# Kernel tuning notes

Hardware: AMD Instinct MI355X
Metric: run time of the kernel (lower is better)

The kernel has to match this reference:

```python
import jax, jax.numpy as jnp
import numpy as np

NUM_NODES = 50000
NUM_EDGES = 800000
IN_DIM = 128
OUT_DIM = 128


def setup_inputs() -> dict:
    key = jax.random.key(0)
    k1, k2, k3 = jax.random.split(key, 3)
    x = jax.random.normal(k1, (NUM_NODES, IN_DIM), dtype=jnp.float32)
    edge_index = jax.random.randint(k2, (2, NUM_EDGES), 0, NUM_NODES, dtype=jnp.int64)
    # xavier_uniform-like init
    limit = float(np.sqrt(6.0 / (IN_DIM + OUT_DIM)))
    weight = jax.random.uniform(k3, (IN_DIM, OUT_DIM), minval=-limit, maxval=limit, dtype=jnp.float32)
    bias = jnp.zeros((OUT_DIM,), dtype=jnp.float32)
    return {"x": x, "edge_index": edge_index, "weight": weight, "bias": bias}


def reference(x, edge_index, weight, bias):
    num_nodes = x.shape[0]
    # add self loops
    self_loops = jnp.broadcast_to(jnp.arange(num_nodes, dtype=edge_index.dtype)[None, :], (2, num_nodes))
    ei = jnp.concatenate([edge_index, self_loops], axis=1)  # [2, E+N]
    row, col = ei[0], ei[1]

    transformed = x @ weight  # [N, out_dim]

    # symmetric normalization: deg counted over source indices (row), as in original
    deg = jax.ops.segment_sum(jnp.ones_like(row, dtype=x.dtype), row, num_segments=num_nodes)
    deg_inv_sqrt = jnp.where(deg > 0, deg ** -0.5, 0.0)
    norm = deg_inv_sqrt[row] * deg_inv_sqrt[col]  # [E+N]

    # gather-scale-scatter: out[dst] += norm * transformed[src]
    messages = norm[:, None] * transformed[row]  # [E+N, out_dim]
    out = jax.ops.segment_sum(messages, col, num_segments=num_nodes)
    return out + bias
```

## Files before the change

### kernel.cpp

```cpp
#include <hip/hip_runtime.h>
#include <hip/hip_fp16.h>


#define EPB 4096

typedef _Float16 f16;
typedef f16 f16x8 __attribute__((ext_vector_type(8)));
typedef float f32x4 __attribute__((ext_vector_type(4)));

static inline int cdiv(int a, int b) { return (a + b - 1) / b; }

__global__ __launch_bounds__(256) void k_hist(const int* __restrict__ ei, int E,
                                              int* __restrict__ hist, int nblk, int nbins,
                                              const float* __restrict__ W,
                                              f16* __restrict__ WhT) {
  __shared__ int ha[256], hb[256];
  const int tid = threadIdx.x, blk = blockIdx.x;
  ha[tid] = 0; hb[tid] = 0;
  __syncthreads();
  const int base = blk * EPB;
  const int lim = min(EPB, E - base);
  if ((E & 3) == 0) {
    for (int i = tid * 4; i + 3 < lim; i += 1024) {
      int4 s4 = *(const int4*)(ei + base + i);
      int4 d4 = *(const int4*)(ei + E + base + i);
      atomicAdd(&ha[d4.x >> 8], 1); atomicAdd(&hb[s4.x >> 8], 1);
      atomicAdd(&ha[d4.y >> 8], 1); atomicAdd(&hb[s4.y >> 8], 1);
      atomicAdd(&ha[d4.z >> 8], 1); atomicAdd(&hb[s4.z >> 8], 1);
      atomicAdd(&ha[d4.w >> 8], 1); atomicAdd(&hb[s4.w >> 8], 1);
    }
    for (int i = (lim & ~3) + tid; i < lim; i += 256) {
      atomicAdd(&ha[ei[E + base + i] >> 8], 1);
      atomicAdd(&hb[ei[base + i] >> 8], 1);
    }
  } else {
    for (int i = tid; i < lim; i += 256) {
      atomicAdd(&ha[ei[E + base + i] >> 8], 1);
      atomicAdd(&hb[ei[base + i] >> 8], 1);
    }
  }
  if (blk < 64) {
    int i = blk * 256 + tid;
    int k = i >> 7, c = i & 127;
    WhT[c * 128 + k] = (f16)W[i];
  }
  __syncthreads();
  if (tid < nbins) {
    hist[tid * nblk + blk] = ha[tid];
    hist[nbins * nblk + tid * nblk + blk] = hb[tid];
  }
}

__global__ __launch_bounds__(256) void k_scan1(int* __restrict__ a,
                                               int* __restrict__ partials, int M) {
  __shared__ int ws[256];
  const int tid = threadIdx.x;
  const int i0 = blockIdx.x * 1024 + tid * 4;
  int v0 = (i0 + 0 < M) ? a[i0 + 0] : 0;
  int v1 = (i0 + 1 < M) ? a[i0 + 1] : 0;
  int v2 = (i0 + 2 < M) ? a[i0 + 2] : 0;
  int v3 = (i0 + 3 < M) ? a[i0 + 3] : 0;
  int tsum = v0 + v1 + v2 + v3;
  ws[tid] = tsum;
  __syncthreads();
#pragma unroll
  for (int off = 1; off < 256; off <<= 1) {
    int add = (tid >= off) ? ws[tid - off] : 0;
    __syncthreads();
    ws[tid] += add;
    __syncthreads();
  }
  int texcl = ws[tid] - tsum;
  if (tid == 255) partials[blockIdx.x] = ws[255];
  if (i0 + 0 < M) a[i0 + 0] = texcl;
  if (i0 + 1 < M) a[i0 + 1] = texcl + v0;
  if (i0 + 2 < M) a[i0 + 2] = texcl + v0 + v1;
  if (i0 + 3 < M) a[i0 + 3] = texcl + v0 + v1 + v2;
}

__device__ __forceinline__ void scan_partials(const int* __restrict__ partials,
                                              int nb1, int* shP, int tid) {
  int v = (tid < nb1) ? partials[tid] : 0;
  shP[tid] = v;
  __syncthreads();
#pragma unroll
  for (int off = 1; off < 256; off <<= 1) {
    int add = (tid >= off) ? shP[tid - off] : 0;
    __syncthreads();
    shP[tid] += add;
    __syncthreads();
  }
  int excl = shP[tid] - v;
  __syncthreads();
  shP[tid] = excl;
  __syncthreads();
}

__global__ __launch_bounds__(256) void k_part(const int* __restrict__ ei, int E,
                                              const int* __restrict__ hist,
                                              const int* __restrict__ partials, int nb1,
                                              int nblk, int nbins,
                                              int* __restrict__ ebA,
                                              unsigned char* __restrict__ ebB) {
  __shared__ int cA[256], cB[256], shP[256];
  const int tid = threadIdx.x, blk = blockIdx.x;
  const int HALF = nbins * nblk;
  scan_partials(partials, nb1, shP, tid);
  if (tid < nbins) {
    int ia = tid * nblk + blk;
    int ib = HALF + tid * nblk + blk;
    cA[tid] = hist[ia] + shP[ia >> 10];
    cB[tid] = hist[ib] + shP[ib >> 10] - E;
  }
  __syncthreads();
  const int base = blk * EPB;
  const int lim = min(EPB, E - base);
  if ((E & 3) == 0) {
    for (int i = tid * 4; i + 3 < lim; i += 1024) {
      int4 s4 = *(const int4*)(ei + base + i);
      int4 d4 = *(const int4*)(ei + E + base + i);
      int pa, pb;
      pa = atomicAdd(&cA[d4.x >> 8], 1); ebA[pa] = (s4.x << 8) | (d4.x & 255);
      pb = atomicAdd(&cB[s4.x >> 8], 1); ebB[pb] = (unsigned char)(s4.x & 255);
      pa = atomicAdd(&cA[d4.y >> 8], 1); ebA[pa] = (s4.y << 8) | (d4.y & 255);
      pb = atomicAdd(&cB[s4.y >> 8], 1); ebB[pb] = (unsigned char)(s4.y & 255);
      pa = atomicAdd(&cA[d4.z >> 8], 1); ebA[pa] = (s4.z << 8) | (d4.z & 255);
      pb = atomicAdd(&cB[s4.z >> 8], 1); ebB[pb] = (unsigned char)(s4.z & 255);
      pa = atomicAdd(&cA[d4.w >> 8], 1); ebA[pa] = (s4.w << 8) | (d4.w & 255);
      pb = atomicAdd(&cB[s4.w >> 8], 1); ebB[pb] = (unsigned char)(s4.w & 255);
    }
    for (int i = (lim & ~3) + tid; i < lim; i += 256) {
      int s = ei[base + i], d = ei[E + base + i];
      int pa = atomicAdd(&cA[d >> 8], 1); ebA[pa] = (s << 8) | (d & 255);
      int pb = atomicAdd(&cB[s >> 8], 1); ebB[pb] = (unsigned char)(s & 255);
    }
  } else {
    for (int i = tid; i < lim; i += 256) {
      int s = ei[base + i], d = ei[E + base + i];
      int pa = atomicAdd(&cA[d >> 8], 1); ebA[pa] = (s << 8) | (d & 255);
      int pb = atomicAdd(&cB[s >> 8], 1); ebB[pb] = (unsigned char)(s & 255);
    }
  }
}

__global__ __launch_bounds__(256) void k_bucket(
    const int* __restrict__ ebA, const unsigned char* __restrict__ ebB,
    const int* __restrict__ hist, const int* __restrict__ partials, int nb1,
    int nblk, int nbins, int E,
    float* __restrict__ dis, int* __restrict__ offs,
    int* __restrict__ srcs, int N) {
  __shared__ int h[256], tmp[256], cur[256], shP[256];
  const int tid = threadIdx.x, b = blockIdx.x;
  const int HALF = nbins * nblk;
  const int node = b * 256 + tid;
  scan_partials(partials, nb1, shP, tid);

  {
    int i0 = HALF + b * nblk;
    const int bs = hist[i0] + shP[i0 >> 10] - E;
    int be = E;
    if (b + 1 < nbins) {
      int i1 = HALF + (b + 1) * nblk;
      be = hist[i1] + shP[i1 >> 10] - E;
    }
    h[tid] = 0;
    __syncthreads();
    for (int j = bs + tid; j < be; j += 256) atomicAdd(&h[ebB[j]], 1);
    __syncthreads();
    if (node < N) dis[node] = rsqrtf(1.0f + (float)h[tid]);
    __syncthreads();
  }

  {
    int i0 = b * nblk;
    const int bs = hist[i0] + shP[i0 >> 10];
    int be = E;
    if (b + 1 < nbins) {
      int i1 = (b + 1) * nblk;
      be = hist[i1] + shP[i1 >> 10];
    }
    h[tid] = 0;
    __syncthreads();
    for (int j = bs + tid; j < be; j += 256) atomicAdd(&h[ebA[j] & 255], 1);
    __syncthreads();
    int cnt = h[tid];
    tmp[tid] = cnt;
    __syncthreads();
#pragma unroll
    for (int off = 1; off < 256; off <<= 1) {
      int add = (tid >= off) ? tmp[tid - off] : 0;
      __syncthreads();
      tmp[tid] += add;
      __syncthreads();
    }
    int gpos = bs + tmp[tid] - cnt;
    if (node < N) offs[node] = gpos;
    cur[tid] = gpos;
    __syncthreads();
    for (int j = bs + tid; j < be; j += 256) {
      int v = ebA[j];
      int p = atomicAdd(&cur[v & 255], 1);
      srcs[p] = (v >> 8) << 6;
    }
    if (b == 0 && tid == 0) offs[N] = E;
  }
}

__global__ __launch_bounds__(256) void k_gemm_mfma(
    const float* __restrict__ x, const f16* __restrict__ WhT,
    const float* __restrict__ dis, __half* __restrict__ t2h, int N) {
  __shared__ __align__(16) f16 cs[4][16][136];
  const int tid = threadIdx.x;
  const int w = tid >> 6, l = tid & 63;
  const int l15 = l & 15, lg = l >> 4;
  const int wr0 = blockIdx.x * 64 + w * 16;
  const int arow = wr0 + l15;
  const bool avalid = arow < N;

  f32x4 acc[8];
#pragma unroll
  for (int ct = 0; ct < 8; ++ct) acc[ct] = (f32x4){0.f, 0.f, 0.f, 0.f};

#pragma unroll
  for (int kc = 0; kc < 4; ++kc) {
    f16x8 af;
    if (avalid) {
      const float4* ap = (const float4*)(x + (size_t)arow * 128 + kc * 32 + lg * 8);
      float4 a0 = ap[0], a1 = ap[1];
      af[0] = (f16)a0.x; af[1] = (f16)a0.y; af[2] = (f16)a0.z; af[3] = (f16)a0.w;
      af[4] = (f16)a1.x; af[5] = (f16)a1.y; af[6] = (f16)a1.z; af[7] = (f16)a1.w;
    } else {
#pragma unroll
      for (int j = 0; j < 8; ++j) af[j] = (f16)0.f;
    }
#pragma unroll
    for (int ct = 0; ct < 8; ++ct) {
      f16x8 bf = *(const f16x8*)(WhT + (ct * 16 + l15) * 128 + kc * 32 + lg * 8);
      acc[ct] = __builtin_amdgcn_mfma_f32_16x16x32_f16(af, bf, acc[ct], 0, 0, 0);
    }
  }

  float d4[4];
#pragma unroll
  for (int j = 0; j < 4; ++j) {
    int r = wr0 + lg * 4 + j;
    d4[j] = (r < N) ? dis[r] : 0.f;
  }
#pragma unroll
  for (int ct = 0; ct < 8; ++ct)
#pragma unroll
    for (int j = 0; j < 4; ++j)
      cs[w][lg * 4 + j][ct * 16 + l15] = (f16)(d4[j] * acc[ct][j]);
  __syncthreads();

#pragma unroll
  for (int it = 0; it < 4; ++it) {
    int t = it * 64 + l;
    int row = t >> 4, seg = t & 15;
    int gr = wr0 + row;
    if (gr < N)
      *(f16x8*)((f16*)t2h + (size_t)gr * 128 + seg * 8) = *(const f16x8*)&cs[w][row][seg * 8];
  }
}

__global__ __launch_bounds__(256) void k_gather(
    const int* __restrict__ offs, const int* __restrict__ srcs,
    const __half* __restrict__ t2h, const float* __restrict__ dis,
    const float* __restrict__ bias, float* __restrict__ out, int N) {
  const int node = blockIdx.x * 4 + (threadIdx.x >> 6);
  const int lane = threadIdx.x & 63;
  if (node >= N) return;

  const int s = offs[node];
  const int e = offs[node + 1];
  const __half2* t2h2 = (const __half2*)t2h;

  float2 acc = __half22float2(t2h2[(size_t)node * 64 + lane]);
  float2 acc2 = make_float2(0.f, 0.f);
  int j = s;
  for (; j + 7 < e; j += 8) {
    int s0 = srcs[j], s1 = srcs[j + 1], s2 = srcs[j + 2], s3 = srcs[j + 3];
    int s4 = srcs[j + 4], s5 = srcs[j + 5], s6 = srcs[j + 6], s7 = srcs[j + 7];
    float2 v0 = __half22float2(t2h2[(size_t)s0 + lane]);
    float2 v1 = __half22float2(t2h2[(size_t)s1 + lane]);
    float2 v2 = __half22float2(t2h2[(size_t)s2 + lane]);
    float2 v3 = __half22float2(t2h2[(size_t)s3 + lane]);
    float2 v4 = __half22float2(t2h2[(size_t)s4 + lane]);
    float2 v5 = __half22float2(t2h2[(size_t)s5 + lane]);
    float2 v6 = __half22float2(t2h2[(size_t)s6 + lane]);
    float2 v7 = __half22float2(t2h2[(size_t)s7 + lane]);
    acc.x += (v0.x + v1.x) + (v2.x + v3.x);
    acc.y += (v0.y + v1.y) + (v2.y + v3.y);
    acc2.x += (v4.x + v5.x) + (v6.x + v7.x);
    acc2.y += (v4.y + v5.y) + (v6.y + v7.y);
  }
  for (; j + 3 < e; j += 4) {
    int s0 = srcs[j], s1 = srcs[j + 1], s2 = srcs[j + 2], s3 = srcs[j + 3];
    float2 v0 = __half22float2(t2h2[(size_t)s0 + lane]);
    float2 v1 = __half22float2(t2h2[(size_t)s1 + lane]);
    float2 v2 = __half22float2(t2h2[(size_t)s2 + lane]);
    float2 v3 = __half22float2(t2h2[(size_t)s3 + lane]);
    acc.x += (v0.x + v1.x) + (v2.x + v3.x);
    acc.y += (v0.y + v1.y) + (v2.y + v3.y);
  }
  for (; j < e; ++j) {
    float2 v = __half22float2(t2h2[(size_t)srcs[j] + lane]);
    acc.x += v.x;
    acc.y += v.y;
  }
  acc.x += acc2.x;
  acc.y += acc2.y;

  const float dn = dis[node];
  const float2 b = *(const float2*)(bias + (size_t)lane * 2);
  float2 r = make_float2(dn * acc.x + b.x, dn * acc.y + b.y);
  *(float2*)(out + (size_t)node * 128 + (size_t)lane * 2) = r;
}

extern "C" void kernel_launch(void* const* d_in, const int* in_sizes, int n_in,
                              void* d_out, int out_size, void* d_ws, size_t ws_size,
                              hipStream_t stream) {
  const float* x = (const float*)d_in[0];
  const int* ei = (const int*)d_in[1];
  const float* W = (const float*)d_in[2];
  const float* bias = (const float*)d_in[3];
  float* out = (float*)d_out;

  const int N = in_sizes[0] / 128;
  const int E = in_sizes[1] / 2;
  const int NBLK = cdiv(E, EPB);
  const int NBINS = cdiv(N, 256);
  const int M = 2 * NBINS * NBLK;
  const int NB1 = cdiv(M, 1024);

  __half* t2h = (__half*)d_ws;
  int* hist = (int*)d_ws;
  int* partials = hist + M;
  int* ebA = partials + 256;
  unsigned char* ebB = (unsigned char*)(ebA + E);
  float* dis = (float*)(t2h + (size_t)N * 128);
  int* offs = (int*)(dis + N);
  int* srcs = offs + (N + 1);
  f16* WhT = (f16*)(srcs + E);

  k_hist<<<NBLK, 256, 0, stream>>>(ei, E, hist, NBLK, NBINS, W, WhT);
  k_scan1<<<NB1, 256, 0, stream>>>(hist, partials, M);
  k_part<<<NBLK, 256, 0, stream>>>(ei, E, hist, partials, NB1, NBLK, NBINS, ebA, ebB);
  k_bucket<<<NBINS, 256, 0, stream>>>(ebA, ebB, hist, partials, NB1, NBLK, NBINS, E,
                                      dis, offs, srcs, N);
  k_gemm_mfma<<<cdiv(N, 64), 256, 0, stream>>>(x, WhT, dis, t2h, N);
  k_gather<<<cdiv(N, 4), 256, 0, stream>>>(offs, srcs, t2h, dis, bias, out, N);
}
```

Baseline: 100.2 us.

## Split gather across column chunks and parallel edge phases with shuffle reduction

The gather kernel now launches eight blocks per group of nodes, and each block handles one 16-column slice of the feature row. Within a wavefront, eight lanes cover the slice while eight lane groups walk different edges in parallel. Partial sums are then combined with xor shuffles. The aim is more independent loads in flight per node, at the cost of each lane group reading only 32 contiguous bytes per source row and each edge list being re-read by eight blocks.

```diff
diff --git a/kernel.cpp b/kernel.cpp
--- a/kernel.cpp
+++ b/kernel.cpp
@@ -267,54 +267,47 @@
     const int* __restrict__ offs, const int* __restrict__ srcs,
     const __half* __restrict__ t2h, const float* __restrict__ dis,
     const float* __restrict__ bias, float* __restrict__ out, int N) {
-  const int node = blockIdx.x * 4 + (threadIdx.x >> 6);
-  const int lane = threadIdx.x & 63;
+  const int k = blockIdx.x & 7;
+  const int g = blockIdx.x >> 3;
+  const int node = g * 4 + (threadIdx.x >> 6);
   if (node >= N) return;
-
-  const int s = offs[node];
-  const int e = offs[node + 1];
-  const __half2* t2h2 = (const __half2*)t2h;
-
-  float2 acc = __half22float2(t2h2[(size_t)node * 64 + lane]);
-  float2 acc2 = make_float2(0.f, 0.f);
-  int j = s;
-  for (; j + 7 < e; j += 8) {
-    int s0 = srcs[j], s1 = srcs[j + 1], s2 = srcs[j + 2], s3 = srcs[j + 3];
-    int s4 = srcs[j + 4], s5 = srcs[j + 5], s6 = srcs[j + 6], s7 = srcs[j + 7];
-    float2 v0 = __half22float2(t2h2[(size_t)s0 + lane]);
-    float2 v1 = __half22float2(t2h2[(size_t)s1 + lane]);
-    float2 v2 = __half22float2(t2h2[(size_t)s2 + lane]);
-    float2 v3 = __half22float2(t2h2[(size_t)s3 + lane]);
-    float2 v4 = __half22float2(t2h2[(size_t)s4 + lane]);
-    float2 v5 = __half22float2(t2h2[(size_t)s5 + lane]);
-    float2 v6 = __half22float2(t2h2[(size_t)s6 + lane]);
-    float2 v7 = __half22float2(t2h2[(size_t)s7 + lane]);
-    acc.x += (v0.x + v1.x) + (v2.x + v3.x);
-    acc.y += (v0.y + v1.y) + (v2.y + v3.y);
-    acc2.x += (v4.x + v5.x) + (v6.x + v7.x);
-    acc2.y += (v4.y + v5.y) + (v6.y + v7.y);
-  }
-  for (; j + 3 < e; j += 4) {
-    int s0 = srcs[j], s1 = srcs[j + 1], s2 = srcs[j + 2], s3 = srcs[j + 3];
-    float2 v0 = __half22float2(t2h2[(size_t)s0 + lane]);
-    float2 v1 = __half22float2(t2h2[(size_t)s1 + lane]);
-    float2 v2 = __half22float2(t2h2[(size_t)s2 + lane]);
-    float2 v3 = __half22float2(t2h2[(size_t)s3 + lane]);
-    acc.x += (v0.x + v1.x) + (v2.x + v3.x);
-    acc.y += (v0.y + v1.y) + (v2.y + v3.y);
-  }
-  for (; j < e; ++j) {
-    float2 v = __half22float2(t2h2[(size_t)srcs[j] + lane]);
-    acc.x += v.x;
-    acc.y += v.y;
-  }
-  acc.x += acc2.x;
-  acc.y += acc2.y;
-
-  const float dn = dis[node];
-  const float2 b = *(const float2*)(bias + (size_t)lane * 2);
-  float2 r = make_float2(dn * acc.x + b.x, dn * acc.y + b.y);
-  *(float2*)(out + (size_t)node * 128 + (size_t)lane * 2) = r;
+  const int l = threadIdx.x & 63;
+  const int ph = l >> 3;
+  const int c = l & 7;
+  const int cb = k * 8 + c;
+  const __half2* t2v = (const __half2*)t2h;
+
+  const int s = offs[node], e = offs[node + 1];
+  float2 acc;
+  if (ph == 0) {
+    acc = __half22float2(t2v[(size_t)node * 64 + cb]);
+  } else {
+    acc = make_float2(0.f, 0.f);
+  }
+  int j = s + ph;
+  for (; j + 8 < e; j += 16) {
+    int s0 = srcs[j], s1 = srcs[j + 8];
+    float2 f0 = __half22float2(t2v[(size_t)s0 + cb]);
+    float2 f1 = __half22float2(t2v[(size_t)s1 + cb]);
+    acc.x += f0.x + f1.x;
+    acc.y += f0.y + f1.y;
+  }
+  if (j < e) {
+    float2 f = __half22float2(t2v[(size_t)srcs[j] + cb]);
+    acc.x += f.x;
+    acc.y += f.y;
+  }
+
+  acc.x += __shfl_xor(acc.x, 8);  acc.y += __shfl_xor(acc.y, 8);
+  acc.x += __shfl_xor(acc.x, 16); acc.y += __shfl_xor(acc.y, 16);
+  acc.x += __shfl_xor(acc.x, 32); acc.y += __shfl_xor(acc.y, 32);
+
+  if (ph == 0) {
+    const float dn = dis[node];
+    const float2 b = *(const float2*)(bias + (size_t)cb * 2);
+    float2 r = make_float2(dn * acc.x + b.x, dn * acc.y + b.y);
+    *(float2*)(out + (size_t)node * 128 + (size_t)cb * 2) = r;
+  }
 }
 
 extern "C" void kernel_launch(void* const* d_in, const int* in_sizes, int n_in,
@@ -349,5 +342,5 @@
   k_bucket<<<NBINS, 256, 0, stream>>>(ebA, ebB, hist, partials, NB1, NBLK, NBINS, E,
                                       dis, offs, srcs, N);
   k_gemm_mfma<<<cdiv(N, 64), 256, 0, stream>>>(x, WhT, dis, t2h, N);
-  k_gather<<<cdiv(N, 4), 256, 0, stream>>>(offs, srcs, t2h, dis, bias, out, N);
-}
+  k_gather<<<cdiv(N, 4) * 8, 256, 0, stream>>>(offs, srcs, t2h, dis, bias, out, N);
+}
```

After: 193.1 us. 1.93x slower.

## Drop separate scan kernel; compute bin offsets redundantly per block and vectorize bucket loops

Applied to the files above, without the earlier changes.

Removes the k_scan1 launch by transposing the histogram layout to block-major and having each k_part and k_bucket block sum the per-bin counts across all partition blocks itself, then run a local scan over bins. This trades one kernel launch and its global round-trip for redundant reads of the small histogram (about 196 blocks × 196 bins) in every block. The bucket kernel's count and scatter loops are also changed to use aligned uchar4/int4 vector loads with head and tail handling. The grid-wide redundant summation adds serial latency per block, up to nblk iterations.

```diff
diff --git a/kernel.cpp b/kernel.cpp
--- a/kernel.cpp
+++ b/kernel.cpp
@@ -16,6 +16,7 @@
                                               f16* __restrict__ WhT) {
   __shared__ int ha[256], hb[256];
   const int tid = threadIdx.x, blk = blockIdx.x;
+  const int HALF = nblk * nbins;
   ha[tid] = 0; hb[tid] = 0;
   __syncthreads();
   const int base = blk * EPB;
@@ -46,73 +47,50 @@
   }
   __syncthreads();
   if (tid < nbins) {
-    hist[tid * nblk + blk] = ha[tid];
-    hist[nbins * nblk + tid * nblk + blk] = hb[tid];
-  }
-}
-
-__global__ __launch_bounds__(256) void k_scan1(int* __restrict__ a,
-                                               int* __restrict__ partials, int M) {
-  __shared__ int ws[256];
-  const int tid = threadIdx.x;
-  const int i0 = blockIdx.x * 1024 + tid * 4;
-  int v0 = (i0 + 0 < M) ? a[i0 + 0] : 0;
-  int v1 = (i0 + 1 < M) ? a[i0 + 1] : 0;
-  int v2 = (i0 + 2 < M) ? a[i0 + 2] : 0;
-  int v3 = (i0 + 3 < M) ? a[i0 + 3] : 0;
-  int tsum = v0 + v1 + v2 + v3;
-  ws[tid] = tsum;
-  __syncthreads();
-#pragma unroll
-  for (int off = 1; off < 256; off <<= 1) {
-    int add = (tid >= off) ? ws[tid - off] : 0;
-    __syncthreads();
-    ws[tid] += add;
-    __syncthreads();
-  }
-  int texcl = ws[tid] - tsum;
-  if (tid == 255) partials[blockIdx.x] = ws[255];
-  if (i0 + 0 < M) a[i0 + 0] = texcl;
-  if (i0 + 1 < M) a[i0 + 1] = texcl + v0;
-  if (i0 + 2 < M) a[i0 + 2] = texcl + v0 + v1;
-  if (i0 + 3 < M) a[i0 + 3] = texcl + v0 + v1 + v2;
-}
-
-__device__ __forceinline__ void scan_partials(const int* __restrict__ partials,
-                                              int nb1, int* shP, int tid) {
-  int v = (tid < nb1) ? partials[tid] : 0;
-  shP[tid] = v;
-  __syncthreads();
-#pragma unroll
-  for (int off = 1; off < 256; off <<= 1) {
-    int add = (tid >= off) ? shP[tid - off] : 0;
-    __syncthreads();
-    shP[tid] += add;
-    __syncthreads();
-  }
-  int excl = shP[tid] - v;
-  __syncthreads();
-  shP[tid] = excl;
-  __syncthreads();
+    hist[blk * nbins + tid] = ha[tid];
+    hist[HALF + blk * nbins + tid] = hb[tid];
+  }
 }
 
 __global__ __launch_bounds__(256) void k_part(const int* __restrict__ ei, int E,
                                               const int* __restrict__ hist,
-                                              const int* __restrict__ partials, int nb1,
                                               int nblk, int nbins,
                                               int* __restrict__ ebA,
                                               unsigned char* __restrict__ ebB) {
-  __shared__ int cA[256], cB[256], shP[256];
+  __shared__ int cA[256], cB[256], sA[256], sB[256];
   const int tid = threadIdx.x, blk = blockIdx.x;
-  const int HALF = nbins * nblk;
-  scan_partials(partials, nb1, shP, tid);
+  const int HALF = nblk * nbins;
+
+  int preA = 0, preB = 0, runA = 0, runB = 0;
   if (tid < nbins) {
-    int ia = tid * nblk + blk;
-    int ib = HALF + tid * nblk + blk;
-    cA[tid] = hist[ia] + shP[ia >> 10];
-    cB[tid] = hist[ib] + shP[ib >> 10] - E;
-  }
-  __syncthreads();
+    for (int j = 0; j < blk; ++j) {
+      preA += hist[j * nbins + tid];
+      preB += hist[HALF + j * nbins + tid];
+    }
+    runA = preA; runB = preB;
+    for (int j = blk; j < nblk; ++j) {
+      runA += hist[j * nbins + tid];
+      runB += hist[HALF + j * nbins + tid];
+    }
+  }
+  sA[tid] = (tid < nbins) ? runA : 0;
+  sB[tid] = (tid < nbins) ? runB : 0;
+  __syncthreads();
+  int vA = sA[tid], vB = sB[tid];
+#pragma unroll
+  for (int off = 1; off < 256; off <<= 1) {
+    int aA = (tid >= off) ? sA[tid - off] : 0;
+    int aB = (tid >= off) ? sB[tid - off] : 0;
+    __syncthreads();
+    sA[tid] += aA; sB[tid] += aB;
+    __syncthreads();
+  }
+  if (tid < nbins) {
+    cA[tid] = (sA[tid] - vA) + preA;
+    cB[tid] = (sB[tid] - vB) + preB;
+  }
+  __syncthreads();
+
   const int base = blk * EPB;
   const int lim = min(EPB, E - base);
   if ((E & 3) == 0) {
@@ -145,43 +123,74 @@
 
 __global__ __launch_bounds__(256) void k_bucket(
     const int* __restrict__ ebA, const unsigned char* __restrict__ ebB,
-    const int* __restrict__ hist, const int* __restrict__ partials, int nb1,
-    int nblk, int nbins, int E,
+    const int* __restrict__ hist, int nblk, int nbins, int E,
     float* __restrict__ dis, int* __restrict__ offs,
     int* __restrict__ srcs, int N) {
-  __shared__ int h[256], tmp[256], cur[256], shP[256];
+  __shared__ int h[256], tmp[256], cur[256];
+  __shared__ int baseA[256], totA[256], baseB[256], totB[256];
   const int tid = threadIdx.x, b = blockIdx.x;
-  const int HALF = nbins * nblk;
+  const int HALF = nblk * nbins;
   const int node = b * 256 + tid;
-  scan_partials(partials, nb1, shP, tid);
+
+  int runA = 0, runB = 0;
+  if (tid < nbins) {
+    for (int j = 0; j < nblk; ++j) {
+      runA += hist[j * nbins + tid];
+      runB += hist[HALF + j * nbins + tid];
+    }
+  }
+  baseA[tid] = (tid < nbins) ? runA : 0;
+  baseB[tid] = (tid < nbins) ? runB : 0;
+  totA[tid] = runA; totB[tid] = runB;
+  __syncthreads();
+  int vA = baseA[tid], vB = baseB[tid];
+#pragma unroll
+  for (int off = 1; off < 256; off <<= 1) {
+    int aA = (tid >= off) ? baseA[tid - off] : 0;
+    int aB = (tid >= off) ? baseB[tid - off] : 0;
+    __syncthreads();
+    baseA[tid] += aA; baseB[tid] += aB;
+    __syncthreads();
+  }
+  baseA[tid] -= vA;
+  baseB[tid] -= vB;
+  __syncthreads();
 
   {
-    int i0 = HALF + b * nblk;
-    const int bs = hist[i0] + shP[i0 >> 10] - E;
-    int be = E;
-    if (b + 1 < nbins) {
-      int i1 = HALF + (b + 1) * nblk;
-      be = hist[i1] + shP[i1 >> 10] - E;
-    }
+    const int bs = baseB[b];
+    const int be = bs + totB[b];
     h[tid] = 0;
     __syncthreads();
-    for (int j = bs + tid; j < be; j += 256) atomicAdd(&h[ebB[j]], 1);
+    int bs_al = (bs + 3) & ~3;
+    if (bs_al > be) bs_al = be;
+    if (tid < bs_al - bs) atomicAdd(&h[ebB[bs + tid]], 1);
+    const int vend = bs_al + ((be - bs_al) & ~3);
+    for (int j = bs_al + tid * 4; j < vend; j += 1024) {
+      uchar4 v = *(const uchar4*)(ebB + j);
+      atomicAdd(&h[v.x], 1); atomicAdd(&h[v.y], 1);
+      atomicAdd(&h[v.z], 1); atomicAdd(&h[v.w], 1);
+    }
+    if (tid < be - vend) atomicAdd(&h[ebB[vend + tid]], 1);
     __syncthreads();
     if (node < N) dis[node] = rsqrtf(1.0f + (float)h[tid]);
     __syncthreads();
   }
 
   {
-    int i0 = b * nblk;
-    const int bs = hist[i0] + shP[i0 >> 10];
-    int be = E;
-    if (b + 1 < nbins) {
-      int i1 = (b + 1) * nblk;
-      be = hist[i1] + shP[i1 >> 10];
-    }
+    const int bs = baseA[b];
+    const int be = bs + totA[b];
     h[tid] = 0;
     __syncthreads();
-    for (int j = bs + tid; j < be; j += 256) atomicAdd(&h[ebA[j] & 255], 1);
+    int bs_al = (bs + 3) & ~3;
+    if (bs_al > be) bs_al = be;
+    if (tid < bs_al - bs) atomicAdd(&h[ebA[bs + tid] & 255], 1);
+    const int vend = bs_al + ((be - bs_al) & ~3);
+    for (int j = bs_al + tid * 4; j < vend; j += 1024) {
+      int4 v = *(const int4*)(ebA + j);
+      atomicAdd(&h[v.x & 255], 1); atomicAdd(&h[v.y & 255], 1);
+      atomicAdd(&h[v.z & 255], 1); atomicAdd(&h[v.w & 255], 1);
+    }
+    if (tid < be - vend) atomicAdd(&h[ebA[vend + tid] & 255], 1);
     __syncthreads();
     int cnt = h[tid];
     tmp[tid] = cnt;
@@ -197,8 +206,21 @@
     if (node < N) offs[node] = gpos;
     cur[tid] = gpos;
     __syncthreads();
-    for (int j = bs + tid; j < be; j += 256) {
-      int v = ebA[j];
+    if (tid < bs_al - bs) {
+      int v = ebA[bs + tid];
+      int p = atomicAdd(&cur[v & 255], 1);
+      srcs[p] = (v >> 8) << 6;
+    }
+    for (int j = bs_al + tid * 4; j < vend; j += 1024) {
+      int4 v = *(const int4*)(ebA + j);
+      int p;
+      p = atomicAdd(&cur[v.x & 255], 1); srcs[p] = (v.x >> 8) << 6;
+      p = atomicAdd(&cur[v.y & 255], 1); srcs[p] = (v.y >> 8) << 6;
+      p = atomicAdd(&cur[v.z & 255], 1); srcs[p] = (v.z >> 8) << 6;
+      p = atomicAdd(&cur[v.w & 255], 1); srcs[p] = (v.w >> 8) << 6;
+    }
+    if (tid < be - vend) {
+      int v = ebA[vend + tid];
       int p = atomicAdd(&cur[v & 255], 1);
       srcs[p] = (v >> 8) << 6;
     }
@@ -273,22 +295,22 @@
 
   const int s = offs[node];
   const int e = offs[node + 1];
-  const __half2* t2h2 = (const __half2*)t2h;
-
-  float2 acc = __half22float2(t2h2[(size_t)node * 64 + lane]);
+  const __half2* t2v = (const __half2*)t2h;
+
+  float2 acc = __half22float2(t2v[(size_t)node * 64 + lane]);
   float2 acc2 = make_float2(0.f, 0.f);
   int j = s;
   for (; j + 7 < e; j += 8) {
     int s0 = srcs[j], s1 = srcs[j + 1], s2 = srcs[j + 2], s3 = srcs[j + 3];
     int s4 = srcs[j + 4], s5 = srcs[j + 5], s6 = srcs[j + 6], s7 = srcs[j + 7];
-    float2 v0 = __half22float2(t2h2[(size_t)s0 + lane]);
-    float2 v1 = __half22float2(t2h2[(size_t)s1 + lane]);
-    float2 v2 = __half22float2(t2h2[(size_t)s2 + lane]);
-    float2 v3 = __half22float2(t2h2[(size_t)s3 + lane]);
-    float2 v4 = __half22float2(t2h2[(size_t)s4 + lane]);
-    float2 v5 = __half22float2(t2h2[(size_t)s5 + lane]);
-    float2 v6 = __half22float2(t2h2[(size_t)s6 + lane]);
-    float2 v7 = __half22float2(t2h2[(size_t)s7 + lane]);
+    float2 v0 = __half22float2(t2v[(size_t)s0 + lane]);
+    float2 v1 = __half22float2(t2v[(size_t)s1 + lane]);
+    float2 v2 = __half22float2(t2v[(size_t)s2 + lane]);
+    float2 v3 = __half22float2(t2v[(size_t)s3 + lane]);
+    float2 v4 = __half22float2(t2v[(size_t)s4 + lane]);
+    float2 v5 = __half22float2(t2v[(size_t)s5 + lane]);
+    float2 v6 = __half22float2(t2v[(size_t)s6 + lane]);
+    float2 v7 = __half22float2(t2v[(size_t)s7 + lane]);
     acc.x += (v0.x + v1.x) + (v2.x + v3.x);
     acc.y += (v0.y + v1.y) + (v2.y + v3.y);
     acc2.x += (v4.x + v5.x) + (v6.x + v7.x);
@@ -296,15 +318,15 @@
   }
   for (; j + 3 < e; j += 4) {
     int s0 = srcs[j], s1 = srcs[j + 1], s2 = srcs[j + 2], s3 = srcs[j + 3];
-    float2 v0 = __half22float2(t2h2[(size_t)s0 + lane]);
-    float2 v1 = __half22float2(t2h2[(size_t)s1 + lane]);
-    float2 v2 = __half22float2(t2h2[(size_t)s2 + lane]);
-    float2 v3 = __half22float2(t2h2[(size_t)s3 + lane]);
+    float2 v0 = __half22float2(t2v[(size_t)s0 + lane]);
+    float2 v1 = __half22float2(t2v[(size_t)s1 + lane]);
+    float2 v2 = __half22float2(t2v[(size_t)s2 + lane]);
+    float2 v3 = __half22float2(t2v[(size_t)s3 + lane]);
     acc.x += (v0.x + v1.x) + (v2.x + v3.x);
     acc.y += (v0.y + v1.y) + (v2.y + v3.y);
   }
   for (; j < e; ++j) {
-    float2 v = __half22float2(t2h2[(size_t)srcs[j] + lane]);
+    float2 v = __half22float2(t2v[(size_t)srcs[j] + lane]);
     acc.x += v.x;
     acc.y += v.y;
   }
@@ -330,13 +352,11 @@
   const int E = in_sizes[1] / 2;
   const int NBLK = cdiv(E, EPB);
   const int NBINS = cdiv(N, 256);
-  const int M = 2 * NBINS * NBLK;
-  const int NB1 = cdiv(M, 1024);
+  const int M = 2 * NBLK * NBINS;
 
   __half* t2h = (__half*)d_ws;
   int* hist = (int*)d_ws;
-  int* partials = hist + M;
-  int* ebA = partials + 256;
+  int* ebA = hist + M;
   unsigned char* ebB = (unsigned char*)(ebA + E);
   float* dis = (float*)(t2h + (size_t)N * 128);
   int* offs = (int*)(dis + N);
@@ -344,9 +364,8 @@
   f16* WhT = (f16*)(srcs + E);
 
   k_hist<<<NBLK, 256, 0, stream>>>(ei, E, hist, NBLK, NBINS, W, WhT);
-  k_scan1<<<NB1, 256, 0, stream>>>(hist, partials, M);
-  k_part<<<NBLK, 256, 0, stream>>>(ei, E, hist, partials, NB1, NBLK, NBINS, ebA, ebB);
-  k_bucket<<<NBINS, 256, 0, stream>>>(ebA, ebB, hist, partials, NB1, NBLK, NBINS, E,
+  k_part<<<NBLK, 256, 0, stream>>>(ei, E, hist, NBLK, NBINS, ebA, ebB);
+  k_bucket<<<NBINS, 256, 0, stream>>>(ebA, ebB, hist, NBLK, NBINS, E,
                                       dis, offs, srcs, N);
   k_gemm_mfma<<<cdiv(N, 64), 256, 0, stream>>>(x, WhT, dis, t2h, N);
   k_gather<<<cdiv(N, 4), 256, 0, stream>>>(offs, srcs, t2h, dis, bias, out, N);
```

New measurement: 168.3 us. 67.9% more time.
